# Performance work log

Measured on AMD Instinct MI355X. Metric: run time of the kernel, lower is better.

The kernel has to match this reference:

```python
import jax, jax.numpy as jnp
import numpy as np

B, C, L, NLAB, EMB, NFREQ, D = 256, 64, 512, 10, 256, 9, 8
FIN, FH, FOUT = 4 * C, C, C
P_TOTAL = FIN * FH + FH + FH * FOUT + FOUT + FIN * FOUT + FOUT


def _leaky(x):
    return jax.nn.leaky_relu(x, 0.2)


def _conv1d(x, w, b=None, pad=0):
    y = jax.lax.conv_general_dilated(x, w, (1,), [(pad, pad)], dimension_numbers=('NCH', 'OIH', 'NCH'))
    return y if b is None else y + b[None, :, None]


def _res1d(x, w0, b0, w1, b1, ws=None, pad=1):
    # GAN-stability style residual block: out = shortcut(x) + 0.1 * conv1(act(conv0(act(x))))
    xs = _conv1d(x, ws) if ws is not None else x
    dx = _conv1d(_leaky(x), w0, b0, pad)
    dx = _conv1d(_leaky(dx), w1, b1, pad)
    return xs + 0.1 * dx


def _pos_enc():
    # sinusoidal positional encoding, 2*NFREQ channels over L positions
    p = np.arange(L, dtype=np.float32)
    f = (np.pi / 2.0 ** np.arange(NFREQ, dtype=np.float32))[:, None]
    pe = np.concatenate([np.sin(f * p), np.cos(f * p)], axis=0)  # [2*NFREQ, L]
    return jnp.asarray(pe)


def _sobel_kernels():
    s = np.array([1.0, 2.0, 1.0], np.float32)
    d = np.array([-1.0, 0.0, 1.0], np.float32)
    kx = np.einsum('i,j,k->ijk', d, s, s)
    ky = np.einsum('i,j,k->ijk', s, d, s)
    kz = np.einsum('i,j,k->ijk', s, s, d)
    return jnp.asarray(np.stack([kx, ky, kz]))  # [3, 3, 3, 3]


def _sin_sobel(x, k):
    # depthwise 3D sobel along each axis, sin of gradients, concat with input -> 4C channels
    outs = [x]
    for i in range(3):
        w = jnp.broadcast_to(k[i][None, None], (C, 1, 3, 3, 3))
        g = jax.lax.conv_general_dilated(x, w, (1, 1, 1), [(1, 1)] * 3,
                                         dimension_numbers=('NCDHW', 'OIDHW', 'NCDHW'),
                                         feature_group_count=C)
        outs.append(jnp.sin(g))
    return jnp.concatenate(outs, axis=1)


def _inst_norm(x):
    m = x.mean(axis=(2, 3, 4), keepdims=True)
    v = x.var(axis=(2, 3, 4), keepdims=True)
    return (x - m) * jax.lax.rsqrt(v + 1e-5)


def _dyna(x, p):
    # hypernet-generated per-sample 1x1x1 residual conv block
    b = x.shape[0]
    xf = x.reshape(b, FIN, D * D * D)
    o = FIN * FH
    wh = p[:, :o].reshape(b, FH, FIN)
    bh = p[:, o:o + FH]; o += FH
    wl = p[:, o:o + FH * FOUT].reshape(b, FOUT, FH); o += FH * FOUT
    bl = p[:, o:o + FOUT]; o += FOUT
    ws = p[:, o:o + FIN * FOUT].reshape(b, FOUT, FIN); o += FIN * FOUT
    bs = p[:, o:o + FOUT]
    xs = jnp.einsum('boi,bis->bos', ws, xf) + bs[:, :, None]
    dx = _leaky(jnp.einsum('bhi,bis->bhs', wh, xf) + bh[:, :, None])
    dx = jnp.einsum('boh,bhs->bos', wl, dx) + bl[:, :, None]
    return (xs + 0.1 * dx).reshape(b, FOUT, D, D, D)


def _forward(codes, y, fc_w, fc_b, in_w0, in_b0, in_w1, in_b1, in_ws, leak, hyper_w, hyper_b,
             out_w0, out_b0, out_w1, out_b1, l1_w0, l1_b0, l1_w1, l1_b1,
             l2_w0, l2_b0, l2_w1, l2_b1, l2_ws):
    b = codes.shape[0]
    yemb = jax.nn.one_hot(y, NLAB, dtype=codes.dtype) @ fc_w.T + fc_b
    yemb = yemb / jnp.maximum(jnp.linalg.norm(yemb, axis=1, keepdims=True), 1e-12)
    pe = jnp.broadcast_to(_pos_enc()[None], (b, 2 * NFREQ, L))
    x = jnp.concatenate([codes, pe], axis=1)  # [B, C+2*NFREQ, L]
    x = _res1d(x, in_w0, in_b0, in_w1, in_b1, ws=in_ws)
    x = x.reshape(b, C, D, D, D)
    leak_c = jnp.clip(leak, 0.001, 1000.0)
    p = yemb @ hyper_w.T + hyper_b  # per-sample dynamic conv params [B, P_TOTAL]
    k = _sobel_kernels()
    for _ in range(8):
        xn = _inst_norm(x)
        xn = _sin_sobel(xn, k)
        xn = _dyna(xn, p)
        x = x + leak_c * xn
    x = x.reshape(b, C, L)
    x = _res1d(x, out_w0, out_b0, out_w1, out_b1)
    code_idx = jnp.argmax(codes, axis=1).reshape(b * L)
    logits = x.transpose(0, 2, 1).reshape(b * L, C)
    logp = jax.nn.log_softmax(logits, axis=-1)
    loss_cent = -jnp.take_along_axis(logp, code_idx[:, None], axis=1).mean()
    lat = _res1d(x, l1_w0, l1_b0, l1_w1, l1_b1, pad=0)
    lat = _res1d(lat, l2_w0, l2_b0, l2_w1, l2_b1, ws=l2_ws, pad=0)
    return lat[:, 0, :], loss_cent


def setup_inputs() -> dict:
    key = jax.random.key(0)
    ks = jax.random.split(key, 16)
    w = lambda k, s: 0.02 * jax.random.normal(k, s, jnp.float32)
    z = lambda s: jnp.zeros(s, jnp.float32)
    CIN = C + 2 * NFREQ  # 82
    return {
        'codes': jax.random.normal(ks[0], (B, C, L), jnp.float32),
        'y': jax.random.randint(ks[1], (B,), 0, NLAB),
        'fc_w': w(ks[2], (EMB, NLAB)), 'fc_b': z((EMB,)),
        'in_w0': w(ks[3], (C, CIN, 3)), 'in_b0': z((C,)),
        'in_w1': w(ks[4], (C, C, 3)), 'in_b1': z((C,)),
        'in_ws': w(ks[5], (C, CIN, 1)),
        'leak': jnp.asarray(0.1, jnp.float32),
        'hyper_w': w(ks[6], (P_TOTAL, EMB)), 'hyper_b': z((P_TOTAL,)),
        'out_w0': w(ks[7], (C, C, 3)), 'out_b0': z((C,)),
        'out_w1': w(ks[8], (C, C, 3)), 'out_b1': z((C,)),
        'l1_w0': w(ks[9], (C, C, 1)), 'l1_b0': z((C,)),
        'l1_w1': w(ks[10], (C, C, 1)), 'l1_b1': z((C,)),
        'l2_w0': w(ks[11], (1, C, 1)), 'l2_b0': z((1,)),
        'l2_w1': w(ks[12], (1, 1, 1)), 'l2_b1': z((1,)),
        'l2_ws': w(ks[13], (1, C, 1)),
    }


def reference(codes, y, fc_w, fc_b, in_w0, in_b0, in_w1, in_b1, in_ws, leak, hyper_w, hyper_b,
              out_w0, out_b0, out_w1, out_b1, l1_w0, l1_b0, l1_w1, l1_b1,
              l2_w0, l2_b0, l2_w1, l2_b1, l2_ws):
    return _forward(codes, y, fc_w, fc_b, in_w0, in_b0, in_w1, in_b1, in_ws, leak, hyper_w, hyper_b,
                    out_w0, out_b0, out_w1, out_b1, l1_w0, l1_b0, l1_w1, l1_b1,
                    l2_w0, l2_b0, l2_w1, l2_b1, l2_ws)
```

## Files before the change

kernel.cpp:

```cpp
#include <hip/hip_runtime.h>

#define B_ 256
#define C_ 64
#define L_ 512
#define CIN_ 82
#define NFREQ_ 9
#define EMB_ 256
#define NLAB_ 10
#define PT_ 37056
#define OFF_BH 16384
#define OFF_WL 16448
#define OFF_BL 20544
#define OFF_WS 20608
#define OFF_BS 36992
#define PI_F 3.14159265358979323846f

typedef short bh8 __attribute__((ext_vector_type(8)));
typedef float f32x4 __attribute__((ext_vector_type(4)));

__device__ inline float lrelu(float v){ return v > 0.f ? v : 0.2f*v; }

__device__ inline unsigned short f2bf(float f){
  unsigned u = __float_as_uint(f);
  u += 0x7FFFu + ((u >> 16) & 1u);
  return (unsigned short)(u >> 16);
}
__device__ inline float bf2f(unsigned short u){
  return __uint_as_float((unsigned)u << 16);
}
__device__ inline unsigned pk2(float a, float b){
  return (unsigned)f2bf(a) | ((unsigned)f2bf(b) << 16);
}
__device__ inline bh8 cvt8(float4 a, float4 b){
  bh8 r;
  r[0]=(short)f2bf(a.x); r[1]=(short)f2bf(a.y); r[2]=(short)f2bf(a.z); r[3]=(short)f2bf(a.w);
  r[4]=(short)f2bf(b.x); r[5]=(short)f2bf(b.y); r[6]=(short)f2bf(b.z); r[7]=(short)f2bf(b.w);
  return r;
}
__device__ inline uint4 pk8(const float* v){
  uint4 o = { pk2(v[0],v[1]), pk2(v[2],v[3]), pk2(v[4],v[5]), pk2(v[6],v[7]) };
  return o;
}
__device__ inline float shf(float v, int a){
  return __uint_as_float((unsigned)__builtin_amdgcn_ds_bpermute(a, (int)__float_as_uint(v)));
}

__global__ __launch_bounds__(256) void k_yemb(const float* __restrict__ fc_w,
    const float* __restrict__ fc_b, const int* __restrict__ y,
    unsigned short* __restrict__ ybf, float* __restrict__ out){
  int b = blockIdx.x, e = threadIdx.x;
  int lab = y[b];
  float v = fc_w[e*NLAB_ + lab] + fc_b[e];
  __shared__ float red[256];
  red[e] = v*v; __syncthreads();
  for (int s = 128; s; s >>= 1){ if (e < s) red[e] += red[e+s]; __syncthreads(); }
  float nrm = fmaxf(sqrtf(red[0]), 1e-12f);
  ybf[(size_t)b*EMB_ + e] = f2bf(v / nrm);
  if (b == 0 && e == 0) out[B_*L_] = 0.f;
}

__global__ __launch_bounds__(256) void k_hyper(const float* __restrict__ hw,
    const float* __restrict__ hb, const unsigned short* __restrict__ ybf,
    unsigned short* __restrict__ p_bf){
  int tid = threadIdx.x;
  int wid = tid >> 6, lane = tid & 63, col = lane & 15, quad = lane >> 4;
  int j = blockIdx.x*64 + wid*16 + col;
  f32x4 acc[16];
  f32x4 z4 = {0.f,0.f,0.f,0.f};
  #pragma unroll
  for (int i = 0; i < 16; i++) acc[i] = z4;
  for (int k0 = 0; k0 < 256; k0 += 32){
    const float* hp = hw + (size_t)j*EMB_ + k0 + quad*8;
    bh8 bf = cvt8(*(const float4*)hp, *(const float4*)(hp+4));
    #pragma unroll
    for (int mt = 0; mt < 16; mt++){
      bh8 af = *(const bh8*)&ybf[(size_t)(mt*16 + col)*EMB_ + k0 + quad*8];
      acc[mt] = __builtin_amdgcn_mfma_f32_16x16x32_bf16(af, bf, acc[mt], 0, 0, 0);
    }
  }
  float hbv = hb[j];
  #pragma unroll
  for (int mt = 0; mt < 16; mt++){
    int b0 = mt*16 + quad*4;
    #pragma unroll
    for (int r = 0; r < 4; r++)
      p_bf[(size_t)(b0 + r)*PT_ + j] = f2bf(acc[mt][r] + hbv);
  }
}

__device__ inline float pe_raw(int fi, int l){
  if (fi < NFREQ_) return __sinf(PI_F / (float)(1 << fi) * (float)l);
  return __cosf(PI_F / (float)(1 << (fi - NFREQ_)) * (float)l);
}

__global__ __launch_bounds__(256) void k_conv_in1(const float* __restrict__ codes,
    const float* __restrict__ w0, const float* __restrict__ b0,
    unsigned short* __restrict__ t1bf){
  int b = blockIdx.x, l0 = blockIdx.y*128, tid = threadIdx.x;
  int wid = tid>>6, lane = tid&63, col = lane&15, quad = lane>>4;
  __shared__ __attribute__((aligned(16))) unsigned short xT[136][96];
  __shared__ __attribute__((aligned(16))) unsigned short wA[3][64][96];
  for (int i = tid; i < 64*96; i += 256){
    int m = i / 96, cin = i % 96;
    if (cin < CIN_){
      const float* s = w0 + (size_t)m*(CIN_*3) + cin*3;
      wA[0][m][cin] = f2bf(s[0]); wA[1][m][cin] = f2bf(s[1]); wA[2][m][cin] = f2bf(s[2]);
    } else { wA[0][m][cin] = 0; wA[1][m][cin] = 0; wA[2][m][cin] = 0; }
  }
  const float* cb = codes + (size_t)b*C_*L_;
  for (int i = tid; i < 96*34; i += 256){
    int c = i / 34, g = i % 34;
    int lg = l0 - 4 + 4*g;
    #pragma unroll
    for (int r2 = 0; r2 < 4; r2++){
      int l = lg + r2;
      float xv = 0.f;
      if (l >= 0 && l < L_){
        if (c < C_) xv = cb[(size_t)c*L_ + l];
        else if (c < CIN_) xv = pe_raw(c - C_, l);
      }
      xT[4*g + r2][c] = f2bf(lrelu(xv));
    }
  }
  __syncthreads();
  f32x4 z4 = {0.f,0.f,0.f,0.f};
  f32x4 acc[8];
  #pragma unroll
  for (int i = 0; i < 8; i++) acc[i] = z4;
  #pragma unroll
  for (int t = 0; t < 3; t++){
    #pragma unroll
    for (int k0 = 0; k0 < 96; k0 += 32){
      bh8 bfr[2];
      #pragma unroll
      for (int nt = 0; nt < 2; nt++)
        bfr[nt] = *(const bh8*)&xT[wid*32 + nt*16 + col + t + 3][k0 + quad*8];
      #pragma unroll
      for (int mt = 0; mt < 4; mt++){
        bh8 af = *(const bh8*)&wA[t][mt*16 + col][k0 + quad*8];
        #pragma unroll
        for (int nt = 0; nt < 2; nt++)
          acc[mt*2+nt] = __builtin_amdgcn_mfma_f32_16x16x32_bf16(af, bfr[nt], acc[mt*2+nt], 0,0,0);
      }
    }
  }
  #pragma unroll
  for (int mt = 0; mt < 4; mt++){
    int f0 = mt*16 + quad*4;
    float q0 = b0[f0], q1 = b0[f0+1], q2 = b0[f0+2], q3 = b0[f0+3];
    #pragma unroll
    for (int nt = 0; nt < 2; nt++){
      int l = l0 + wid*32 + nt*16 + col;
      f32x4 a = acc[mt*2+nt];
      uint2 o = { pk2(lrelu(a[0]+q0), lrelu(a[1]+q1)),
                  pk2(lrelu(a[2]+q2), lrelu(a[3]+q3)) };
      *(uint2*)&t1bf[((size_t)b*L_ + l)*64 + f0] = o;
    }
  }
}

__global__ __launch_bounds__(256) void k_conv_in2(const float* __restrict__ codes,
    const float* __restrict__ wsp, const float* __restrict__ w1, const float* __restrict__ b1,
    const unsigned short* __restrict__ t1bf, float* __restrict__ x){
  int b = blockIdx.x, l0 = blockIdx.y*128, tid = threadIdx.x;
  int wid = tid>>6, lane = tid&63, col = lane&15, quad = lane>>4;
  __shared__ __attribute__((aligned(16))) unsigned short xT[128][96];
  __shared__ __attribute__((aligned(16))) unsigned short wsA[64][96];
  __shared__ __attribute__((aligned(16))) unsigned short w1A[3][64][72];
  for (int i = tid; i < 64*96; i += 256){
    int m = i / 96, cin = i % 96;
    wsA[m][cin] = (cin < CIN_) ? f2bf(wsp[(size_t)m*CIN_ + cin]) : (unsigned short)0;
  }
  for (int i = tid; i < 64*64; i += 256){
    int m = i >> 6, cin = i & 63;
    const float* s = w1 + (size_t)m*192 + cin*3;
    w1A[0][m][cin] = f2bf(s[0]); w1A[1][m][cin] = f2bf(s[1]); w1A[2][m][cin] = f2bf(s[2]);
  }
  const float* cb = codes + (size_t)b*C_*L_;
  for (int i = tid; i < 96*32; i += 256){
    int c = i / 32, g = i % 32;
    int lg = l0 + 4*g;
    #pragma unroll
    for (int r2 = 0; r2 < 4; r2++){
      int l = lg + r2;
      float xv;
      if (c < C_) xv = cb[(size_t)c*L_ + l];
      else if (c < CIN_) xv = pe_raw(c - C_, l);
      else xv = 0.f;
      xT[4*g + r2][c] = f2bf(xv);
    }
  }
  __syncthreads();
  f32x4 z4 = {0.f,0.f,0.f,0.f};
  f32x4 accS[8], accD[8];
  #pragma unroll
  for (int i = 0; i < 8; i++){ accS[i] = z4; accD[i] = z4; }
  #pragma unroll
  for (int k0 = 0; k0 < 96; k0 += 32){
    bh8 bfr[2];
    #pragma unroll
    for (int nt = 0; nt < 2; nt++)
      bfr[nt] = *(const bh8*)&xT[wid*32 + nt*16 + col][k0 + quad*8];
    #pragma unroll
    for (int mt = 0; mt < 4; mt++){
      bh8 af = *(const bh8*)&wsA[mt*16 + col][k0 + quad*8];
      #pragma unroll
      for (int nt = 0; nt < 2; nt++)
        accS[mt*2+nt] = __builtin_amdgcn_mfma_f32_16x16x32_bf16(af, bfr[nt], accS[mt*2+nt], 0,0,0);
    }
  }
  bh8 zz8 = {0,0,0,0,0,0,0,0};
  #pragma unroll
  for (int t = 0; t < 3; t++){
    #pragma unroll
    for (int k0 = 0; k0 < 64; k0 += 32){
      bh8 bfr[2];
      #pragma unroll
      for (int nt = 0; nt < 2; nt++){
        int l = l0 + wid*32 + nt*16 + col + t - 1;
        bfr[nt] = (l >= 0 && l < L_)
          ? *(const bh8*)&t1bf[((size_t)b*L_ + l)*64 + k0 + quad*8] : zz8;
      }
      #pragma unroll
      for (int mt = 0; mt < 4; mt++){
        bh8 af = *(const bh8*)&w1A[t][mt*16 + col][k0 + quad*8];
        #pragma unroll
        for (int nt = 0; nt < 2; nt++)
          accD[mt*2+nt] = __builtin_amdgcn_mfma_f32_16x16x32_bf16(af, bfr[nt], accD[mt*2+nt], 0,0,0);
      }
    }
  }
  #pragma unroll
  for (int mt = 0; mt < 4; mt++){
    int f0 = mt*16 + quad*4;
    float q0 = b1[f0], q1 = b1[f0+1], q2 = b1[f0+2], q3 = b1[f0+3];
    #pragma unroll
    for (int nt = 0; nt < 2; nt++){
      int l = l0 + wid*32 + nt*16 + col;
      f32x4 s = accS[mt*2+nt], d = accD[mt*2+nt];
      size_t base = ((size_t)b*C_ + f0)*L_ + l;
      x[base]        = s[0] + 0.1f*(d[0] + q0);
      x[base + L_]   = s[1] + 0.1f*(d[1] + q1);
      x[base + 2*L_] = s[2] + 0.1f*(d[2] + q2);
      x[base + 3*L_] = s[3] + 0.1f*(d[3] + q3);
    }
  }
}

#define GSTR 16408
__global__ __launch_bounds__(512, 2) void k_loop(float* __restrict__ x,
    const unsigned short* __restrict__ p_bf, const float* __restrict__ leak){
  const int b = blockIdx.x, tid = threadIdx.x;
  const int wid = tid >> 6, lane = tid & 63, col = lane & 15, quad = lane >> 4;
  const int yy = lane & 7, zz = lane >> 3;
  const unsigned short* pb = p_bf + (size_t)b*PT_;
  float* xb = x + (size_t)b*C_*L_;

  __shared__ __attribute__((aligned(16))) unsigned short Tbuf[4*GSTR];
  unsigned short (*h_t)[72] = (unsigned short (*)[72])Tbuf;

  const int lmA = ((yy > 0) ? lane-1 : lane)*4;  const float wm = (yy > 0) ? 1.f : 0.f;
  const int lpA = ((yy < 7) ? lane+1 : lane)*4;  const float wp = (yy < 7) ? 1.f : 0.f;
  const int zmA = ((zz > 0) ? lane-8 : lane)*4;  const float qm = (zz > 0) ? 1.f : 0.f;
  const int zpA = ((zz < 7) ? lane+8 : lane)*4;  const float qp = (zz < 7) ? 1.f : 0.f;

  const float lk = fminf(fmaxf(leak[0], 0.001f), 1000.f);
  const f32x4 z4 = {0.f,0.f,0.f,0.f};

  for (int it = 0; it < 8; ++it){
    f32x4 acc1[32];
    #pragma unroll
    for (int i = 0; i < 32; i++) acc1[i] = z4;

    #pragma unroll 1
    for (int h = 0; h < 2; ++h){
      const float* xr0 = xb + (size_t)(h*32 + wid)*L_ + lane*8;
      float4 nv0 = *(const float4*)xr0, nv1 = *(const float4*)(xr0 + 4);
      #pragma unroll 1
      for (int c4 = 0; c4 < 4; ++c4){
        const int chl = c4*8 + wid;
        float r[8] = {nv0.x,nv0.y,nv0.z,nv0.w,nv1.x,nv1.y,nv1.z,nv1.w};
        if (c4 < 3){
          const float* xr = xb + (size_t)(h*32 + (c4+1)*8 + wid)*L_ + lane*8;
          nv0 = *(const float4*)xr; nv1 = *(const float4*)(xr + 4);
        }
        float s1 = 0.f, s2 = 0.f;
        #pragma unroll
        for (int i = 0; i < 8; i++){ s1 += r[i]; s2 += r[i]*r[i]; }
        #pragma unroll
        for (int m = 32; m; m >>= 1){ s1 += __shfl_xor(s1, m); s2 += __shfl_xor(s2, m); }
        const float mean = s1 * (1.f/512.f);
        const float rstd = rsqrtf(s2*(1.f/512.f) - mean*mean + 1e-5f);
        float xn[8];
        #pragma unroll
        for (int i = 0; i < 8; i++) xn[i] = (r[i]-mean)*rstd;
        *(uint4*)&Tbuf[chl*512 + lane*8] = pk8(xn);
        float A[8], Bv[8];
        A[0] = 2.f*xn[0]+xn[1]; Bv[0] = xn[1];
        #pragma unroll
        for (int i = 1; i < 7; i++){ A[i] = xn[i-1]+2.f*xn[i]+xn[i+1]; Bv[i] = xn[i+1]-xn[i-1]; }
        A[7] = xn[6]+2.f*xn[7]; Bv[7] = -xn[6];
        float Cv[8], Dv[8], Ev[8];
        #pragma unroll
        for (int i = 0; i < 8; i++){
          float am = shf(A[i], lmA)*wm, ap = shf(A[i], lpA)*wp;
          Cv[i] = am + 2.f*A[i] + ap;
          Dv[i] = ap - am;
          float bm = shf(Bv[i], lmA)*wm, bp = shf(Bv[i], lpA)*wp;
          Ev[i] = bm + 2.f*Bv[i] + bp;
        }
        float g0[8], g1[8], g2[8];
        #pragma unroll
        for (int i = 0; i < 8; i++){
          g0[i] = __sinf(shf(Cv[i], zpA)*qp - shf(Cv[i], zmA)*qm);
          g1[i] = __sinf(shf(Dv[i], zmA)*qm + 2.f*Dv[i] + shf(Dv[i], zpA)*qp);
          g2[i] = __sinf(shf(Ev[i], zmA)*qm + 2.f*Ev[i] + shf(Ev[i], zpA)*qp);
        }
        *(uint4*)&Tbuf[GSTR   + chl*512 + lane*8] = pk8(g0);
        *(uint4*)&Tbuf[2*GSTR + chl*512 + lane*8] = pk8(g1);
        *(uint4*)&Tbuf[3*GSTR + chl*512 + lane*8] = pk8(g2);
      }
      __syncthreads();
      #pragma unroll
      for (int kt = 0; kt < 4; ++kt){
        bh8 bfr[4];
        #pragma unroll
        for (int nt = 0; nt < 4; nt++){
          const int n = wid*64 + nt*16 + col;
          bh8 fv;
          #pragma unroll
          for (int j = 0; j < 8; j++) fv[j] = (short)Tbuf[quad*GSTR + (kt*8+j)*512 + n];
          bfr[nt] = fv;
        }
        const int kof = quad*64 + h*32 + kt*8;
        #pragma unroll
        for (int mt = 0; mt < 8; mt++){
          bh8 af = (mt < 4)
            ? *(const bh8*)&pb[(size_t)(mt*16+col)*256 + kof]
            : *(const bh8*)&pb[OFF_WS + (size_t)((mt-4)*16+col)*256 + kof];
          #pragma unroll
          for (int nt = 0; nt < 4; nt++)
            acc1[mt*4+nt] = __builtin_amdgcn_mfma_f32_16x16x32_bf16(af, bfr[nt], acc1[mt*4+nt], 0,0,0);
        }
      }
      __syncthreads();
    }

    #pragma unroll
    for (int mt = 0; mt < 4; mt++){
      const int f0 = mt*16 + quad*4;
      const float bh0 = bf2f(pb[OFF_BH+f0]),   bh1 = bf2f(pb[OFF_BH+f0+1]);
      const float bh2 = bf2f(pb[OFF_BH+f0+2]), bh3 = bf2f(pb[OFF_BH+f0+3]);
      #pragma unroll
      for (int nt = 0; nt < 4; nt++){
        const int n = wid*64 + nt*16 + col;
        f32x4 a = acc1[mt*4+nt];
        uint2 o = { pk2(lrelu(a[0]+bh0), lrelu(a[1]+bh1)),
                    pk2(lrelu(a[2]+bh2), lrelu(a[3]+bh3)) };
        *(uint2*)&h_t[n][f0] = o;
      }
    }
    f32x4 acc2[16];
    #pragma unroll
    for (int i = 0; i < 16; i++) acc2[i] = z4;
    #pragma unroll
    for (int k0 = 0; k0 < 64; k0 += 32){
      bh8 hb[4];
      #pragma unroll
      for (int nt = 0; nt < 4; nt++)
        hb[nt] = *(const bh8*)&h_t[wid*64 + nt*16 + col][k0 + quad*8];
      #pragma unroll
      for (int mt = 0; mt < 4; mt++){
        bh8 al = *(const bh8*)&pb[OFF_WL + (size_t)(mt*16 + col)*64 + k0 + quad*8];
        #pragma unroll
        for (int nt = 0; nt < 4; nt++)
          acc2[mt*4+nt] = __builtin_amdgcn_mfma_f32_16x16x32_bf16(al, hb[nt], acc2[mt*4+nt], 0,0,0);
      }
    }
    #pragma unroll
    for (int mt = 0; mt < 4; mt++){
      const int f0 = mt*16 + quad*4;
      const float bs0 = bf2f(pb[OFF_BS+f0]),   bs1 = bf2f(pb[OFF_BS+f0+1]);
      const float bs2 = bf2f(pb[OFF_BS+f0+2]), bs3 = bf2f(pb[OFF_BS+f0+3]);
      const float bl0 = bf2f(pb[OFF_BL+f0]),   bl1 = bf2f(pb[OFF_BL+f0+1]);
      const float bl2 = bf2f(pb[OFF_BL+f0+2]), bl3 = bf2f(pb[OFF_BL+f0+3]);
      #pragma unroll
      for (int nt = 0; nt < 4; nt++){
        const int n = wid*64 + nt*16 + col;
        f32x4 xs = acc1[(mt+4)*4+nt], dx = acc2[mt*4+nt];
        size_t xi = (size_t)f0*L_ + n;
        xb[xi]        += lk*(xs[0] + bs0 + 0.1f*(dx[0] + bl0));
        xb[xi + L_]   += lk*(xs[1] + bs1 + 0.1f*(dx[1] + bl1));
        xb[xi + 2*L_] += lk*(xs[2] + bs2 + 0.1f*(dx[2] + bl2));
        xb[xi + 3*L_] += lk*(xs[3] + bs3 + 0.1f*(dx[3] + bl3));
      }
    }
    __threadfence_block();
    __syncthreads();
  }
}

__global__ __launch_bounds__(256) void k_conv_out1(const float* __restrict__ x,
    const float* __restrict__ w, const float* __restrict__ bias,
    unsigned short* __restrict__ t1bf){
  int b = blockIdx.x, l0 = blockIdx.y*128, tid = threadIdx.x;
  int wid = tid>>6, lane = tid&63, col = lane&15, quad = lane>>4;
  __shared__ __attribute__((aligned(16))) unsigned short xT[136][72];
  __shared__ __attribute__((aligned(16))) unsigned short wA[3][64][72];
  for (int i = tid; i < 64*64; i += 256){
    int m = i >> 6, cin = i & 63;
    const float* s = w + (size_t)m*192 + cin*3;
    wA[0][m][cin] = f2bf(s[0]); wA[1][m][cin] = f2bf(s[1]); wA[2][m][cin] = f2bf(s[2]);
  }
  const float* xb = x + (size_t)b*C_*L_;
  for (int i = tid; i < 64*34; i += 256){
    int c = i / 34, g = i % 34;
    int lg = l0 - 4 + 4*g;
    if (lg >= 0 && lg + 3 < L_){
      float4 f = *(const float4*)&xb[(size_t)c*L_ + lg];
      xT[4*g  ][c] = f2bf(lrelu(f.x));
      xT[4*g+1][c] = f2bf(lrelu(f.y));
      xT[4*g+2][c] = f2bf(lrelu(f.z));
      xT[4*g+3][c] = f2bf(lrelu(f.w));
    } else {
      #pragma unroll
      for (int r2 = 0; r2 < 4; r2++){
        int l = lg + r2;
        float v = (l >= 0 && l < L_) ? xb[(size_t)c*L_ + l] : 0.f;
        xT[4*g + r2][c] = f2bf(lrelu(v));
      }
    }
  }
  __syncthreads();
  f32x4 z4 = {0.f,0.f,0.f,0.f};
  f32x4 acc[8];
  #pragma unroll
  for (int i = 0; i < 8; i++) acc[i] = z4;
  #pragma unroll
  for (int t = 0; t < 3; t++){
    #pragma unroll
    for (int k0 = 0; k0 < 64; k0 += 32){
      bh8 bfr[2];
      #pragma unroll
      for (int nt = 0; nt < 2; nt++)
        bfr[nt] = *(const bh8*)&xT[wid*32 + nt*16 + col + t + 3][k0 + quad*8];
      #pragma unroll
      for (int mt = 0; mt < 4; mt++){
        bh8 af = *(const bh8*)&wA[t][mt*16 + col][k0 + quad*8];
        #pragma unroll
        for (int nt = 0; nt < 2; nt++)
          acc[mt*2+nt] = __builtin_amdgcn_mfma_f32_16x16x32_bf16(af, bfr[nt], acc[mt*2+nt], 0,0,0);
      }
    }
  }
  #pragma unroll
  for (int mt = 0; mt < 4; mt++){
    int f0 = mt*16 + quad*4;
    float q0 = bias[f0], q1 = bias[f0+1], q2 = bias[f0+2], q3 = bias[f0+3];
    #pragma unroll
    for (int nt = 0; nt < 2; nt++){
      int l = l0 + wid*32 + nt*16 + col;
      f32x4 a = acc[mt*2+nt];
      uint2 o = { pk2(lrelu(a[0]+q0), lrelu(a[1]+q1)),
                  pk2(lrelu(a[2]+q2), lrelu(a[3]+q3)) };
      *(uint2*)&t1bf[((size_t)b*L_ + l)*64 + f0] = o;
    }
  }
}

__global__ __launch_bounds__(256) void k_conv_out2(float* __restrict__ x,
    const unsigned short* __restrict__ t1bf, const float* __restrict__ w,
    const float* __restrict__ bias){
  int b = blockIdx.x, l0 = blockIdx.y*256, tid = threadIdx.x;
  int wid = tid>>6, lane = tid&63, col = lane&15, quad = lane>>4;
  __shared__ __attribute__((aligned(16))) unsigned short wA[3][64][72];
  for (int i = tid; i < 64*64; i += 256){
    int m = i >> 6, cin = i & 63;
    const float* s = w + (size_t)m*192 + cin*3;
    wA[0][m][cin] = f2bf(s[0]); wA[1][m][cin] = f2bf(s[1]); wA[2][m][cin] = f2bf(s[2]);
  }
  __syncthreads();
  f32x4 z4 = {0.f,0.f,0.f,0.f};
  f32x4 acc[16];
  #pragma unroll
  for (int i = 0; i < 16; i++) acc[i] = z4;
  bh8 zz8 = {0,0,0,0,0,0,0,0};
  #pragma unroll
  for (int t = 0; t < 3; t++){
    #pragma unroll
    for (int k0 = 0; k0 < 64; k0 += 32){
      bh8 bfr[4];
      #pragma unroll
      for (int nt = 0; nt < 4; nt++){
        int l = l0 + wid*64 + nt*16 + col + t - 1;
        bfr[nt] = (l >= 0 && l < L_)
          ? *(const bh8*)&t1bf[((size_t)b*L_ + l)*64 + k0 + quad*8] : zz8;
      }
      #pragma unroll
      for (int mt = 0; mt < 4; mt++){
        bh8 af = *(const bh8*)&wA[t][mt*16 + col][k0 + quad*8];
        #pragma unroll
        for (int nt = 0; nt < 4; nt++)
          acc[mt*4+nt] = __builtin_amdgcn_mfma_f32_16x16x32_bf16(af, bfr[nt], acc[mt*4+nt], 0,0,0);
      }
    }
  }
  #pragma unroll
  for (int mt = 0; mt < 4; mt++){
    int f0 = mt*16 + quad*4;
    float q0 = bias[f0], q1 = bias[f0+1], q2 = bias[f0+2], q3 = bias[f0+3];
    #pragma unroll
    for (int nt = 0; nt < 4; nt++){
      int l = l0 + wid*64 + nt*16 + col;
      f32x4 a = acc[mt*4+nt];
      size_t base = ((size_t)b*C_ + f0)*L_ + l;
      x[base]        += 0.1f*(a[0] + q0);
      x[base + L_]   += 0.1f*(a[1] + q1);
      x[base + 2*L_] += 0.1f*(a[2] + q2);
      x[base + 3*L_] += 0.1f*(a[3] + q3);
    }
  }
}

__global__ __launch_bounds__(256) void k_loss(const float* __restrict__ x,
    const float* __restrict__ codes, float* __restrict__ out){
  int b = blockIdx.x;
  int l = blockIdx.y*256 + threadIdx.x;
  const float* xb = x + (size_t)b*C_*L_ + l;
  const float* cb = codes + (size_t)b*C_*L_ + l;
  float m = -1e30f, cm = -1e30f;
  int ci = 0;
  for (int c = 0; c < C_; c++){
    float xv = xb[(size_t)c*L_];
    m = fmaxf(m, xv);
    float cv = cb[(size_t)c*L_];
    if (cv > cm){ cm = cv; ci = c; }
  }
  float s = 0.f, vi = 0.f;
  for (int c = 0; c < C_; c++){
    float xv = xb[(size_t)c*L_];
    s += expf(xv - m);
    if (c == ci) vi = xv;
  }
  float lp = vi - m - logf(s);
  __shared__ float red[256];
  red[threadIdx.x] = -lp; __syncthreads();
  for (int sft = 128; sft; sft >>= 1){
    if (threadIdx.x < sft) red[threadIdx.x] += red[threadIdx.x + sft];
    __syncthreads();
  }
  if (threadIdx.x == 0) atomicAdd(out + B_*L_, red[0] * (1.0f/131072.0f));
}

__global__ __launch_bounds__(256) void k_lat(const float* __restrict__ x,
    const float* __restrict__ w10, const float* __restrict__ b10,
    const float* __restrict__ w11, const float* __restrict__ b11,
    const float* __restrict__ w20, const float* __restrict__ b20,
    const float* __restrict__ w21, const float* __restrict__ b21,
    const float* __restrict__ ws2, float* __restrict__ out){
  int b = blockIdx.x, l0 = blockIdx.y*256;
  int tid = threadIdx.x;
  int wid = tid >> 6, lane = tid & 63, col = lane & 15, quad = lane >> 4;
  __shared__ __attribute__((aligned(16))) unsigned short wA[2][64][72];
  __shared__ __attribute__((aligned(16))) unsigned short Bt[256][72];

  for (int i = tid; i < 1024; i += 256){
    int arr = i >> 9, rem = i & 511, row = rem >> 3, seg = rem & 7;
    const float* src = (arr ? w11 : w10) + (size_t)row*C_ + seg*8;
    *(bh8*)&wA[arr][row][seg*8] = cvt8(*(const float4*)src, *(const float4*)(src+4));
  }
  for (int i = tid; i < 4096; i += 256){
    int c = i >> 6, seg = i & 63;
    float4 v = *(const float4*)&x[((size_t)b*C_ + c)*L_ + l0 + seg*4];
    Bt[seg*4+0][c] = f2bf(lrelu(v.x));
    Bt[seg*4+1][c] = f2bf(lrelu(v.y));
    Bt[seg*4+2][c] = f2bf(lrelu(v.z));
    Bt[seg*4+3][c] = f2bf(lrelu(v.w));
  }
  __syncthreads();
  f32x4 z4 = {0.f,0.f,0.f,0.f};
  f32x4 acc1[16];
  #pragma unroll
  for (int i = 0; i < 16; i++) acc1[i] = z4;
  #pragma unroll
  for (int k0 = 0; k0 < 64; k0 += 32){
    bh8 bfr[4];
    #pragma unroll
    for (int nt = 0; nt < 4; nt++)
      bfr[nt] = *(const bh8*)&Bt[wid*64 + nt*16 + col][k0 + quad*8];
    #pragma unroll
    for (int mt = 0; mt < 4; mt++){
      bh8 af = *(const bh8*)&wA[0][mt*16 + col][k0 + quad*8];
      #pragma unroll
      for (int nt = 0; nt < 4; nt++)
        acc1[mt*4+nt] = __builtin_amdgcn_mfma_f32_16x16x32_bf16(af, bfr[nt], acc1[mt*4+nt], 0, 0, 0);
    }
  }
  #pragma unroll
  for (int mt = 0; mt < 4; mt++){
    int f0 = mt*16 + quad*4;
    f32x4 bv = *(const f32x4*)&b10[f0];
    #pragma unroll
    for (int nt = 0; nt < 4; nt++){
      int n = wid*64 + nt*16 + col;
      f32x4 a = acc1[mt*4+nt];
      uint2 o = { pk2(lrelu(a[0]+bv[0]), lrelu(a[1]+bv[1])),
                  pk2(lrelu(a[2]+bv[2]), lrelu(a[3]+bv[3])) };
      *(uint2*)&Bt[n][f0] = o;
    }
  }
  f32x4 acc2[16];
  #pragma unroll
  for (int i = 0; i < 16; i++) acc2[i] = z4;
  #pragma unroll
  for (int k0 = 0; k0 < 64; k0 += 32){
    bh8 bfr[4];
    #pragma unroll
    for (int nt = 0; nt < 4; nt++)
      bfr[nt] = *(const bh8*)&Bt[wid*64 + nt*16 + col][k0 + quad*8];
    #pragma unroll
    for (int mt = 0; mt < 4; mt++){
      bh8 af = *(const bh8*)&wA[1][mt*16 + col][k0 + quad*8];
      #pragma unroll
      for (int nt = 0; nt < 4; nt++)
        acc2[mt*4+nt] = __builtin_amdgcn_mfma_f32_16x16x32_bf16(af, bfr[nt], acc2[mt*4+nt], 0, 0, 0);
    }
  }
  float psA[4] = {0.f,0.f,0.f,0.f}, psB[4] = {0.f,0.f,0.f,0.f};
  #pragma unroll
  for (int mt = 0; mt < 4; mt++){
    int f0 = mt*16 + quad*4;
    f32x4 b11v = *(const f32x4*)&b11[f0];
    f32x4 wsv  = *(const f32x4*)&ws2[f0];
    f32x4 w20v = *(const f32x4*)&w20[f0];
    #pragma unroll
    for (int nt = 0; nt < 4; nt++){
      int lg = l0 + wid*64 + nt*16 + col;
      size_t base = ((size_t)b*C_ + f0)*L_ + lg;
      f32x4 a = acc2[mt*4+nt];
      #pragma unroll
      for (int r = 0; r < 4; r++){
        float xv = x[base + (size_t)r*L_];
        float lat = xv + 0.1f*(a[r] + b11v[r]);
        psA[nt] += wsv[r]*lat;
        psB[nt] += w20v[r]*lrelu(lat);
      }
    }
  }
  #pragma unroll
  for (int nt = 0; nt < 4; nt++){
    psA[nt] += __shfl_xor(psA[nt], 16); psA[nt] += __shfl_xor(psA[nt], 32);
    psB[nt] += __shfl_xor(psB[nt], 16); psB[nt] += __shfl_xor(psB[nt], 32);
  }
  if (quad == 0){
    float b20s = b20[0], w21s = w21[0], b21s = b21[0];
    #pragma unroll
    for (int nt = 0; nt < 4; nt++){
      float dx2 = w21s*lrelu(psB[nt] + b20s) + b21s;
      out[(size_t)b*L_ + l0 + wid*64 + nt*16 + col] = psA[nt] + 0.1f*dx2;
    }
  }
}

extern "C" void kernel_launch(void* const* d_in, const int* in_sizes, int n_in,
                              void* d_out, int out_size, void* d_ws, size_t ws_size,
                              hipStream_t stream) {
  (void)in_sizes; (void)n_in; (void)out_size; (void)ws_size;
  const float* codes   = (const float*)d_in[0];
  const int*   y       = (const int*)  d_in[1];
  const float* fc_w    = (const float*)d_in[2];
  const float* fc_b    = (const float*)d_in[3];
  const float* in_w0   = (const float*)d_in[4];
  const float* in_b0   = (const float*)d_in[5];
  const float* in_w1   = (const float*)d_in[6];
  const float* in_b1   = (const float*)d_in[7];
  const float* in_wsp  = (const float*)d_in[8];
  const float* leak    = (const float*)d_in[9];
  const float* hyper_w = (const float*)d_in[10];
  const float* hyper_b = (const float*)d_in[11];
  const float* out_w0  = (const float*)d_in[12];
  const float* out_b0  = (const float*)d_in[13];
  const float* out_w1  = (const float*)d_in[14];
  const float* out_b1  = (const float*)d_in[15];
  const float* l1_w0   = (const float*)d_in[16];
  const float* l1_b0   = (const float*)d_in[17];
  const float* l1_w1   = (const float*)d_in[18];
  const float* l1_b1   = (const float*)d_in[19];
  const float* l2_w0   = (const float*)d_in[20];
  const float* l2_b0   = (const float*)d_in[21];
  const float* l2_w1   = (const float*)d_in[22];
  const float* l2_b1   = (const float*)d_in[23];
  const float* l2_ws   = (const float*)d_in[24];
  float* out = (float*)d_out;

  char* ws = (char*)d_ws;
  unsigned short* p_bf = (unsigned short*)(ws);
  unsigned short* ybf  = (unsigned short*)(ws + 18972672);
  float* x             = (float*)(ws + 19103744);
  unsigned short* t1bf = (unsigned short*)(ws + 52658176);

  k_yemb<<<B_, 256, 0, stream>>>(fc_w, fc_b, y, ybf, out);
  k_hyper<<<PT_/64, 256, 0, stream>>>(hyper_w, hyper_b, ybf, p_bf);
  k_conv_in1<<<dim3(B_, 4), 256, 0, stream>>>(codes, in_w0, in_b0, t1bf);
  k_conv_in2<<<dim3(B_, 4), 256, 0, stream>>>(codes, in_wsp, in_w1, in_b1, t1bf, x);
  k_loop<<<B_, 512, 0, stream>>>(x, p_bf, leak);
  k_conv_out1<<<dim3(B_, 4), 256, 0, stream>>>(x, out_w0, out_b0, t1bf);
  k_conv_out2<<<dim3(B_, 2), 256, 0, stream>>>(x, t1bf, out_w1, out_b1);
  k_loss<<<dim3(B_, 2), 256, 0, stream>>>(x, codes, out);
  k_lat<<<dim3(B_, 2), 256, 0, stream>>>(x, l1_w0, l1_b0, l1_w1, l1_b1,
                                         l2_w0, l2_b0, l2_w1, l2_b1, l2_ws, out);
}
```

Measured before the change: 908.8 us.

## Keep loop state in registers across iterations, exchange updates via LDS

The 8-iteration k_loop now loads each sample's 64x512 activation tile into registers once and keeps it there. Each iteration's residual update is staged through shared memory and accumulated into the registers, instead of doing read-modify-write on global memory every iteration. The result is written back to global memory only once at the end. Launch bounds drop to one block per CU to make room for the extra 64 floats per thread, which lowers occupancy and adds two more block barriers per iteration.

```diff
diff --git a/kernel.cpp b/kernel.cpp
--- a/kernel.cpp
+++ b/kernel.cpp
@@ -17,6 +17,7 @@
 
 typedef short bh8 __attribute__((ext_vector_type(8)));
 typedef float f32x4 __attribute__((ext_vector_type(4)));
+typedef float f32x8 __attribute__((ext_vector_type(8)));
 
 __device__ inline float lrelu(float v){ return v > 0.f ? v : 0.2f*v; }
 
@@ -248,7 +249,47 @@
 }
 
 #define GSTR 16408
-__global__ __launch_bounds__(512, 2) void k_loop(float* __restrict__ x,
+#define CHUNK(G) { \
+      f32x8 r = xr[G]; \
+      float s1 = 0.f, s2 = 0.f; \
+      _Pragma("unroll") \
+      for (int i = 0; i < 8; i++){ s1 += r[i]; s2 += r[i]*r[i]; } \
+      _Pragma("unroll") \
+      for (int m = 32; m; m >>= 1){ s1 += __shfl_xor(s1, m); s2 += __shfl_xor(s2, m); } \
+      const float mean = s1 * (1.f/512.f); \
+      const float rstd = rsqrtf(s2*(1.f/512.f) - mean*mean + 1e-5f); \
+      const int toff = (((G)&3)*8 + wid)*512 + lane*8; \
+      float xn[8]; \
+      _Pragma("unroll") \
+      for (int i = 0; i < 8; i++) xn[i] = (r[i]-mean)*rstd; \
+      *(uint4*)&Tbuf[toff] = pk8(xn); \
+      float A[8], Bv[8]; \
+      A[0] = 2.f*xn[0]+xn[1]; Bv[0] = xn[1]; \
+      _Pragma("unroll") \
+      for (int i = 1; i < 7; i++){ A[i] = xn[i-1]+2.f*xn[i]+xn[i+1]; Bv[i] = xn[i+1]-xn[i-1]; } \
+      A[7] = xn[6]+2.f*xn[7]; Bv[7] = -xn[6]; \
+      float Cv[8], Dv[8], Ev[8]; \
+      _Pragma("unroll") \
+      for (int i = 0; i < 8; i++){ \
+        float am = shf(A[i], lmA)*wm, ap = shf(A[i], lpA)*wp; \
+        Cv[i] = am + 2.f*A[i] + ap; \
+        Dv[i] = ap - am; \
+        float bm = shf(Bv[i], lmA)*wm, bp = shf(Bv[i], lpA)*wp; \
+        Ev[i] = bm + 2.f*Bv[i] + bp; \
+      } \
+      float g0[8], g1[8], g2[8]; \
+      _Pragma("unroll") \
+      for (int i = 0; i < 8; i++){ \
+        g0[i] = __sinf(shf(Cv[i], zpA)*qp - shf(Cv[i], zmA)*qm); \
+        g1[i] = __sinf(shf(Dv[i], zmA)*qm + 2.f*Dv[i] + shf(Dv[i], zpA)*qp); \
+        g2[i] = __sinf(shf(Ev[i], zmA)*qm + 2.f*Ev[i] + shf(Ev[i], zpA)*qp); \
+      } \
+      *(uint4*)&Tbuf[GSTR   + toff] = pk8(g0); \
+      *(uint4*)&Tbuf[2*GSTR + toff] = pk8(g1); \
+      *(uint4*)&Tbuf[3*GSTR + toff] = pk8(g2); \
+    }
+
+__global__ __launch_bounds__(512, 1) void k_loop(float* __restrict__ x,
     const unsigned short* __restrict__ p_bf, const float* __restrict__ leak){
   const int b = blockIdx.x, tid = threadIdx.x;
   const int wid = tid >> 6, lane = tid & 63, col = lane & 15, quad = lane >> 4;
@@ -258,6 +299,7 @@
 
   __shared__ __attribute__((aligned(16))) unsigned short Tbuf[4*GSTR];
   unsigned short (*h_t)[72] = (unsigned short (*)[72])Tbuf;
+  float* U = (float*)Tbuf;
 
   const int lmA = ((yy > 0) ? lane-1 : lane)*4;  const float wm = (yy > 0) ? 1.f : 0.f;
   const int lpA = ((yy < 7) ? lane+1 : lane)*4;  const float wp = (yy < 7) ? 1.f : 0.f;
@@ -267,59 +309,24 @@
   const float lk = fminf(fmaxf(leak[0], 0.001f), 1000.f);
   const f32x4 z4 = {0.f,0.f,0.f,0.f};
 
+  f32x8 xr[8];
+  #pragma unroll
+  for (int g = 0; g < 8; g++){
+    const float* s = xb + (size_t)(g*8 + wid)*L_ + lane*8;
+    float4 a = *(const float4*)s, c = *(const float4*)(s + 4);
+    f32x8 v = {a.x,a.y,a.z,a.w,c.x,c.y,c.z,c.w};
+    xr[g] = v;
+  }
+
   for (int it = 0; it < 8; ++it){
     f32x4 acc1[32];
     #pragma unroll
     for (int i = 0; i < 32; i++) acc1[i] = z4;
 
-    #pragma unroll 1
+    #pragma unroll
     for (int h = 0; h < 2; ++h){
-      const float* xr0 = xb + (size_t)(h*32 + wid)*L_ + lane*8;
-      float4 nv0 = *(const float4*)xr0, nv1 = *(const float4*)(xr0 + 4);
-      #pragma unroll 1
-      for (int c4 = 0; c4 < 4; ++c4){
-        const int chl = c4*8 + wid;
-        float r[8] = {nv0.x,nv0.y,nv0.z,nv0.w,nv1.x,nv1.y,nv1.z,nv1.w};
-        if (c4 < 3){
-          const float* xr = xb + (size_t)(h*32 + (c4+1)*8 + wid)*L_ + lane*8;
-          nv0 = *(const float4*)xr; nv1 = *(const float4*)(xr + 4);
-        }
-        float s1 = 0.f, s2 = 0.f;
-        #pragma unroll
-        for (int i = 0; i < 8; i++){ s1 += r[i]; s2 += r[i]*r[i]; }
-        #pragma unroll
-        for (int m = 32; m; m >>= 1){ s1 += __shfl_xor(s1, m); s2 += __shfl_xor(s2, m); }
-        const float mean = s1 * (1.f/512.f);
-        const float rstd = rsqrtf(s2*(1.f/512.f) - mean*mean + 1e-5f);
-        float xn[8];
-        #pragma unroll
-        for (int i = 0; i < 8; i++) xn[i] = (r[i]-mean)*rstd;
-        *(uint4*)&Tbuf[chl*512 + lane*8] = pk8(xn);
-        float A[8], Bv[8];
-        A[0] = 2.f*xn[0]+xn[1]; Bv[0] = xn[1];
-        #pragma unroll
-        for (int i = 1; i < 7; i++){ A[i] = xn[i-1]+2.f*xn[i]+xn[i+1]; Bv[i] = xn[i+1]-xn[i-1]; }
-        A[7] = xn[6]+2.f*xn[7]; Bv[7] = -xn[6];
-        float Cv[8], Dv[8], Ev[8];
-        #pragma unroll
-        for (int i = 0; i < 8; i++){
-          float am = shf(A[i], lmA)*wm, ap = shf(A[i], lpA)*wp;
-          Cv[i] = am + 2.f*A[i] + ap;
-          Dv[i] = ap - am;
-          float bm = shf(Bv[i], lmA)*wm, bp = shf(Bv[i], lpA)*wp;
-          Ev[i] = bm + 2.f*Bv[i] + bp;
-        }
-        float g0[8], g1[8], g2[8];
-        #pragma unroll
-        for (int i = 0; i < 8; i++){
-          g0[i] = __sinf(shf(Cv[i], zpA)*qp - shf(Cv[i], zmA)*qm);
-          g1[i] = __sinf(shf(Dv[i], zmA)*qm + 2.f*Dv[i] + shf(Dv[i], zpA)*qp);
-          g2[i] = __sinf(shf(Ev[i], zmA)*qm + 2.f*Ev[i] + shf(Ev[i], zpA)*qp);
-        }
-        *(uint4*)&Tbuf[GSTR   + chl*512 + lane*8] = pk8(g0);
-        *(uint4*)&Tbuf[2*GSTR + chl*512 + lane*8] = pk8(g1);
-        *(uint4*)&Tbuf[3*GSTR + chl*512 + lane*8] = pk8(g2);
-      }
+      if (h == 0){ CHUNK(0) CHUNK(1) CHUNK(2) CHUNK(3) }
+      else       { CHUNK(4) CHUNK(5) CHUNK(6) CHUNK(7) }
       __syncthreads();
       #pragma unroll
       for (int kt = 0; kt < 4; ++kt){
@@ -377,6 +384,7 @@
           acc2[mt*4+nt] = __builtin_amdgcn_mfma_f32_16x16x32_bf16(al, hb[nt], acc2[mt*4+nt], 0,0,0);
       }
     }
+    __syncthreads();
     #pragma unroll
     for (int mt = 0; mt < 4; mt++){
       const int f0 = mt*16 + quad*4;
@@ -386,17 +394,31 @@
       const float bl2 = bf2f(pb[OFF_BL+f0+2]), bl3 = bf2f(pb[OFF_BL+f0+3]);
       #pragma unroll
       for (int nt = 0; nt < 4; nt++){
-        const int n = wid*64 + nt*16 + col;
+        const int s = wid*64 + nt*16 + col;
         f32x4 xs = acc1[(mt+4)*4+nt], dx = acc2[mt*4+nt];
-        size_t xi = (size_t)f0*L_ + n;
-        xb[xi]        += lk*(xs[0] + bs0 + 0.1f*(dx[0] + bl0));
-        xb[xi + L_]   += lk*(xs[1] + bs1 + 0.1f*(dx[1] + bl1));
-        xb[xi + 2*L_] += lk*(xs[2] + bs2 + 0.1f*(dx[2] + bl2));
-        xb[xi + 3*L_] += lk*(xs[3] + bs3 + 0.1f*(dx[3] + bl3));
-      }
-    }
-    __threadfence_block();
+        U[(size_t)(f0+0)*512 + s] = lk*(xs[0] + bs0 + 0.1f*(dx[0] + bl0));
+        U[(size_t)(f0+1)*512 + s] = lk*(xs[1] + bs1 + 0.1f*(dx[1] + bl1));
+        U[(size_t)(f0+2)*512 + s] = lk*(xs[2] + bs2 + 0.1f*(dx[2] + bl2));
+        U[(size_t)(f0+3)*512 + s] = lk*(xs[3] + bs3 + 0.1f*(dx[3] + bl3));
+      }
+    }
     __syncthreads();
+    #pragma unroll
+    for (int g = 0; g < 8; g++){
+      const float* us = &U[(size_t)(g*8 + wid)*512 + lane*8];
+      float4 a = *(const float4*)us, c = *(const float4*)(us + 4);
+      f32x8 add = {a.x,a.y,a.z,a.w,c.x,c.y,c.z,c.w};
+      xr[g] += add;
+    }
+    __syncthreads();
+  }
+
+  #pragma unroll
+  for (int g = 0; g < 8; g++){
+    float* s = xb + (size_t)(g*8 + wid)*L_ + lane*8;
+    f32x8 v = xr[g];
+    float4 a = {v[0],v[1],v[2],v[3]}, c = {v[4],v[5],v[6],v[7]};
+    *(float4*)s = a; *(float4*)(s + 4) = c;
   }
 }
 
```

Result: slower. 1.125 ms (+23.8%).
